# Kernel tuning notes

Measured on AMD Instinct MI355X. Metric: run time of the kernel, lower is better.

## Reference

```python
import jax, jax.numpy as jnp
import numpy as np

HIDDEN = 1024
HEADS = 16
HEAD_DIM = HIDDEN // HEADS
EPS = 1e-6


def _layernorm(x, gamma, beta):
    mu = jnp.mean(x, axis=-1, keepdims=True)
    var = jnp.mean(jnp.square(x - mu), axis=-1, keepdims=True)
    return (x - mu) * jax.lax.rsqrt(var + EPS) * gamma + beta


def setup_inputs() -> dict:
    key = jax.random.key(0)
    ks = jax.random.split(key, 16)
    B, S, D = 2, 2048, HIDDEN
    s = 1.0 / np.sqrt(D)
    inp = {
        "x": jax.random.normal(ks[0], (B, S, D), dtype=jnp.float32),
        "Wq": jax.random.uniform(ks[1], (D, D), jnp.float32, -s, s),
        "bq": jnp.zeros((D,), jnp.float32),
        "Wk": jax.random.uniform(ks[2], (D, D), jnp.float32, -s, s),
        "bk": jnp.zeros((D,), jnp.float32),
        "Wv": jax.random.uniform(ks[3], (D, D), jnp.float32, -s, s),
        "bv": jnp.zeros((D,), jnp.float32),
        "Wo": jax.random.uniform(ks[4], (D, D), jnp.float32, -s, s),
        "bo": jnp.zeros((D,), jnp.float32),
        "g1": jnp.ones((D,), jnp.float32),
        "b1": jnp.zeros((D,), jnp.float32),
        "Wup": jax.random.uniform(ks[5], (D, 4 * D), jnp.float32, -s, s),
        "bup": jnp.zeros((4 * D,), jnp.float32),
        "Wdn": jax.random.uniform(ks[6], (4 * D, D), jnp.float32, -0.5 * s, 0.5 * s),
        "bdn": jnp.zeros((D,), jnp.float32),
        "g2": jnp.ones((D,), jnp.float32),
        "b2": jnp.zeros((D,), jnp.float32),
    }
    return inp


def _forward(x, Wq, bq, Wk, bk, Wv, bv, Wo, bo, g1, b1, Wup, bup, Wdn, bdn, g2, b2):
    B, S, D = x.shape
    H, Hd = HEADS, HEAD_DIM
    # projections -> (B, H, S, Hd)
    q = (x @ Wq + bq).reshape(B, S, H, Hd).transpose(0, 2, 1, 3)
    k = (x @ Wk + bk).reshape(B, S, H, Hd).transpose(0, 2, 1, 3)
    v = (x @ Wv + bv).reshape(B, S, H, Hd).transpose(0, 2, 1, 3)
    # full NxN scores (faithful to the source: explicit QK^T, mask, softmax, AV)
    scores = jnp.einsum("bhqd,bhkd->bhqk", q, k) / np.sqrt(Hd)
    causal = jnp.tril(jnp.ones((S, S), dtype=bool))  # (S, S)
    scores = jnp.where(causal, scores, jnp.float32(-1e20))
    attn = jax.nn.softmax(scores, axis=-1)
    # dropout is identity in eval mode
    mid = jnp.einsum("bhqk,bhkd->bqhd", attn, v).reshape(B, S, D)
    attn_out = mid @ Wo + bo
    x = _layernorm(x + attn_out, g1, b1)
    # FFN
    up = jax.nn.relu(x @ Wup + bup)
    down = up @ Wdn + bdn
    return _layernorm(x + down, g2, b2)


def reference(x, Wq, bq, Wk, bk, Wv, bv, Wo, bo, g1, b1, Wup, bup, Wdn, bdn, g2, b2):
    return _forward(x, Wq, bq, Wk, bk, Wv, bv, Wo, bo, g1, b1, Wup, bup, Wdn, bdn, g2, b2)
```

## Files before the change

kernel.cpp:

```cpp
#include <hip/hip_runtime.h>

#define D_MODEL 1024
#define D_FFN   4096
#define SEQ     2048
#define NROWS   4096
#define QKV_LD  3072

typedef __bf16 bf16x8 __attribute__((ext_vector_type(8)));
typedef float  floatx4 __attribute__((ext_vector_type(4)));

#define MFMA_BF16 __builtin_amdgcn_mfma_f32_16x16x32_bf16

__device__ __forceinline__ unsigned short f2bf(float f) {
  unsigned int u = __float_as_uint(f);
  u += 0x7FFFu + ((u >> 16) & 1u);
  return (unsigned short)(u >> 16);
}

template <int C>
__device__ __forceinline__ float ror16(float x) {
  return __int_as_float(
      __builtin_amdgcn_mov_dpp(__float_as_int(x), 0x120 | C, 0xf, 0xf, true));
}

__device__ __forceinline__ void async16(const unsigned short* g, unsigned short* l) {
  __builtin_amdgcn_global_load_lds(
      (const __attribute__((address_space(1))) unsigned int*)g,
      (__attribute__((address_space(3))) unsigned int*)l, 16, 0, 0);
}

__global__ __launch_bounds__(256) void k_f32_to_bf16(
    const float* __restrict__ in, unsigned short* __restrict__ outp, long n) {
  long i = ((long)blockIdx.x * 256 + threadIdx.x) * 4;
  if (i >= n) return;
  float4 v = *(const float4*)(in + i);
  ushort4 o;
  o.x = f2bf(v.x); o.y = f2bf(v.y); o.z = f2bf(v.z); o.w = f2bf(v.w);
  *(ushort4*)(outp + i) = o;
}

__global__ __launch_bounds__(256) void k_transpose_bf16(
    const float* __restrict__ W, unsigned short* __restrict__ WT, int R, int C) {
  __shared__ float tile[32][33];
  int tx = threadIdx.x & 31, ty = threadIdx.x >> 5;
  long bx = (long)blockIdx.x * 32;
  long by = (long)blockIdx.y * 32;
  #pragma unroll
  for (int j = 0; j < 4; j++)
    tile[ty + j * 8][tx] = W[(by + ty + j * 8) * C + bx + tx];
  __syncthreads();
  #pragma unroll
  for (int j = 0; j < 4; j++)
    WT[(bx + ty + j * 8) * R + by + tx] = f2bf(tile[tx][ty + j * 8]);
}

__global__ __launch_bounds__(256) void k_transpose_sq(
    const float* __restrict__ Wq, const float* __restrict__ Wk,
    const float* __restrict__ Wv, const float* __restrict__ Wo,
    unsigned short* __restrict__ WqkvT, unsigned short* __restrict__ WoT) {
  __shared__ float tile[32][33];
  int z = blockIdx.z;
  const float* W = (z == 0) ? Wq : (z == 1) ? Wk : (z == 2) ? Wv : Wo;
  unsigned short* dst = (z < 3) ? (WqkvT + (size_t)z * D_MODEL * D_MODEL) : WoT;
  int tx = threadIdx.x & 31, ty = threadIdx.x >> 5;
  long bx = (long)blockIdx.x * 32;
  long by = (long)blockIdx.y * 32;
  #pragma unroll
  for (int j = 0; j < 4; j++)
    tile[ty + j * 8][tx] = W[(by + ty + j * 8) * D_MODEL + bx + tx];
  __syncthreads();
  #pragma unroll
  for (int j = 0; j < 4; j++)
    dst[(bx + ty + j * 8) * D_MODEL + by + tx] = f2bf(tile[tx][ty + j * 8]);
}

__global__ __launch_bounds__(256) void k_pack_bias(
    const float* __restrict__ bq, const float* __restrict__ bk,
    const float* __restrict__ bv, float* __restrict__ dst) {
  int i = blockIdx.x * 256 + threadIdx.x;
  if (i >= 3072) return;
  float v = (i < 1024) ? bq[i] : (i < 2048) ? bk[i - 1024] : bv[i - 2048];
  dst[i] = v;
}

__global__ __launch_bounds__(256) void k_transpose_v(
    const unsigned short* __restrict__ QKV, unsigned short* __restrict__ Vt) {
  __shared__ unsigned short tile[64][72];
  int r0 = blockIdx.x * 64;
  int c0 = blockIdx.y * 64;
  int tx = threadIdx.x & 15, ty = threadIdx.x >> 4;
  #pragma unroll
  for (int j = 0; j < 4; j++) {
    int r = ty + j * 16;
    *(ushort4*)&tile[r][tx * 4] =
        *(const ushort4*)(QKV + (long)(r0 + r) * QKV_LD + 2048 + c0 + tx * 4);
  }
  __syncthreads();
  #pragma unroll
  for (int j = 0; j < 4; j++) {
    int d = ty + j * 16;
    ushort4 o;
    o.x = tile[tx * 4 + 0][d];
    o.y = tile[tx * 4 + 1][d];
    o.z = tile[tx * 4 + 2][d];
    o.w = tile[tx * 4 + 3][d];
    *(ushort4*)(Vt + (long)(c0 + d) * NROWS + r0 + tx * 4) = o;
  }
}

__global__ __launch_bounds__(512, 4) void k_gemm128(
    const unsigned short* __restrict__ A,
    const unsigned short* __restrict__ Bt,
    const float* __restrict__ bias,
    void* __restrict__ Cp, int M, int N, int K, int flags) {
  __shared__ unsigned short lds[2 * 16384];
  int tid = threadIdx.x, lane = tid & 63, wave = tid >> 6;
  int quad = lane >> 4, l16 = lane & 15;
  int wm = wave >> 2, wn = wave & 3;

  int gx = gridDim.x;
  int nwg = gx * gridDim.y;
  int orig = blockIdx.y * gx + blockIdx.x;
  int wg = (orig & 7) * (nwg >> 3) + (orig >> 3);
  long bm = (long)(wg % gx) * 128;
  long bn = (long)(wg / gx) * 128;

  int T = K / 64;

  const floatx4 fz = {0.f, 0.f, 0.f, 0.f};
  floatx4 acc[4][2];
  #pragma unroll
  for (int i = 0; i < 4; i++)
    #pragma unroll
    for (int j = 0; j < 2; j++) acc[i][j] = fz;

  int srow = tid >> 3;
  int sc = (tid & 7) ^ (srow & 7);
  const unsigned short* Ag = A + (bm + srow) * (long)K + sc * 8;
  const unsigned short* Bg = Bt + (bn + srow) * (long)K + sc * 8;

  auto stage = [&](int tt, int c) {
    unsigned short* An = lds + c * 16384;
    unsigned short* Bn = An + 8192;
    long ko = (long)tt * 64;
    async16(Ag + ko, An + wave * 512);
    async16(Ag + 64 * (long)K + ko, An + 4096 + wave * 512);
    async16(Bg + ko, Bn + wave * 512);
    async16(Bg + 64 * (long)K + ko, Bn + 4096 + wave * 512);
  };

  int aoff = (wm * 64 + l16) * 64;
  int boff = (wn * 32 + l16) * 64;
  int sw = l16 & 7;
  int ca0 = (quad ^ sw) * 8;
  int ca1 = ((4 + quad) ^ sw) * 8;

  stage(0, 0);
  for (int t = 0; t < T; t++) {
    int c = t & 1;
    const unsigned short* Ac = lds + c * 16384;
    const unsigned short* Bc = Ac + 8192;
    int tn = (t + 1 < T) ? t + 1 : T - 1;
    stage(tn, c ^ 1);
    __asm__ volatile("s_waitcnt vmcnt(4)" ::: "memory");
    __builtin_amdgcn_s_barrier();

    bf16x8 af[4][2], bfr[2][2];
    #pragma unroll
    for (int m = 0; m < 4; m++) {
      af[m][0] = *(const bf16x8*)(Ac + aoff + m * 1024 + ca0);
      af[m][1] = *(const bf16x8*)(Ac + aoff + m * 1024 + ca1);
    }
    #pragma unroll
    for (int n = 0; n < 2; n++) {
      bfr[n][0] = *(const bf16x8*)(Bc + boff + n * 1024 + ca0);
      bfr[n][1] = *(const bf16x8*)(Bc + boff + n * 1024 + ca1);
    }
    __asm__ volatile("s_waitcnt lgkmcnt(0)" ::: "memory");
    __builtin_amdgcn_s_setprio(1);
    #pragma unroll
    for (int h = 0; h < 2; h++)
      #pragma unroll
      for (int m = 0; m < 4; m++)
        #pragma unroll
        for (int n = 0; n < 2; n++)
          acc[m][n] = MFMA_BF16(af[m][h], bfr[n][h], acc[m][n], 0, 0, 0);
    __builtin_amdgcn_s_setprio(0);
    __builtin_amdgcn_s_barrier();
  }

  bool f32out = (flags & 1) != 0;
  bool relu   = (flags & 2) != 0;
  float* outf = (float*)Cp;
  unsigned short* outh = (unsigned short*)Cp;
  #pragma unroll
  for (int n = 0; n < 2; n++) {
    long col = bn + wn * 32 + n * 16 + l16;
    float bvv = bias[col];
    #pragma unroll
    for (int m = 0; m < 4; m++) {
      long row = bm + wm * 64 + m * 16 + quad * 4;
      #pragma unroll
      for (int r = 0; r < 4; r++) {
        float v = acc[m][n][r] + bvv;
        if (relu) v = fmaxf(v, 0.0f);
        if (f32out) outf[(row + r) * (long)N + col] = v;
        else        outh[(row + r) * (long)N + col] = f2bf(v);
      }
    }
  }
}

__global__ __launch_bounds__(512, 2) void k_gemm256(
    const unsigned short* __restrict__ A,
    const unsigned short* __restrict__ Bt,
    const float* __restrict__ bias,
    void* __restrict__ Cp, int M, int N, int K, int flags) {
  extern __shared__ unsigned short lds[];
  int tid = threadIdx.x, lane = tid & 63, wave = tid >> 6;
  int quad = lane >> 4, l16 = lane & 15;
  int wm = wave >> 2, wn = wave & 3;

  int nwg = gridDim.x * gridDim.y;
  int orig = blockIdx.y * gridDim.x + blockIdx.x;
  int wg = (orig & 7) * (nwg >> 3) + (orig >> 3);
  long bm = (long)(wg & 15) * 256;
  long bn = (long)(wg >> 4) * 256;

  int z = blockIdx.z;
  int Ks = K / gridDim.z;
  long zb = (long)z * Ks;
  int T = Ks / 64;

  const floatx4 fz = {0.f, 0.f, 0.f, 0.f};
  floatx4 acc[8][4];
  #pragma unroll
  for (int i = 0; i < 8; i++)
    #pragma unroll
    for (int j = 0; j < 4; j++) acc[i][j] = fz;

  int srow = tid >> 3;
  int sc = (tid & 7) ^ (srow & 7);
  const unsigned short* Ag = A + (bm + srow) * (long)K + zb + sc * 8;
  const unsigned short* Bg = Bt + (bn + srow) * (long)K + zb + sc * 8;

  auto stage = [&](int tt, int c) {
    unsigned short* An = lds + c * 32768;
    unsigned short* Bn = An + 16384;
    long ko = (long)tt * 64;
    #pragma unroll
    for (int i = 0; i < 4; i++) {
      async16(Ag + (long)i * 64 * K + ko, An + i * 4096 + wave * 512);
      async16(Bg + (long)i * 64 * K + ko, Bn + i * 4096 + wave * 512);
    }
  };

  int aoff = (wm * 128 + l16) * 64;
  int boff = (wn * 64 + l16) * 64;
  int sw = l16 & 7;
  int ca0 = (quad ^ sw) * 8;
  int ca1 = ((4 + quad) ^ sw) * 8;

  stage(0, 0);
  for (int t = 0; t < T; t++) {
    int c = t & 1;
    const unsigned short* Ac = lds + c * 32768;
    const unsigned short* Bc = Ac + 16384;
    int tn = (t + 1 < T) ? t + 1 : T - 1;
    stage(tn, c ^ 1);
    __asm__ volatile("s_waitcnt vmcnt(8)" ::: "memory");
    __builtin_amdgcn_s_barrier();

    bf16x8 af[8], b0, b1;
    #pragma unroll
    for (int m = 0; m < 8; m++) af[m] = *(const bf16x8*)(Ac + aoff + m * 1024 + ca0);
    b0 = *(const bf16x8*)(Bc + boff + 0 * 1024 + ca0);
    b1 = *(const bf16x8*)(Bc + boff + 1 * 1024 + ca0);
    __asm__ volatile("s_waitcnt lgkmcnt(0)" ::: "memory");
    __builtin_amdgcn_s_setprio(1);
    #pragma unroll
    for (int m = 0; m < 8; m++) acc[m][0] = MFMA_BF16(af[m], b0, acc[m][0], 0, 0, 0);
    #pragma unroll
    for (int m = 0; m < 8; m++) acc[m][1] = MFMA_BF16(af[m], b1, acc[m][1], 0, 0, 0);
    __builtin_amdgcn_s_setprio(0);
    __builtin_amdgcn_s_barrier();
    b0 = *(const bf16x8*)(Bc + boff + 2 * 1024 + ca0);
    b1 = *(const bf16x8*)(Bc + boff + 3 * 1024 + ca0);
    __asm__ volatile("s_waitcnt lgkmcnt(0)" ::: "memory");
    __builtin_amdgcn_s_setprio(1);
    #pragma unroll
    for (int m = 0; m < 8; m++) acc[m][2] = MFMA_BF16(af[m], b0, acc[m][2], 0, 0, 0);
    #pragma unroll
    for (int m = 0; m < 8; m++) acc[m][3] = MFMA_BF16(af[m], b1, acc[m][3], 0, 0, 0);
    __builtin_amdgcn_s_setprio(0);
    __builtin_amdgcn_s_barrier();
    #pragma unroll
    for (int m = 0; m < 8; m++) af[m] = *(const bf16x8*)(Ac + aoff + m * 1024 + ca1);
    b0 = *(const bf16x8*)(Bc + boff + 0 * 1024 + ca1);
    b1 = *(const bf16x8*)(Bc + boff + 1 * 1024 + ca1);
    __asm__ volatile("s_waitcnt lgkmcnt(0)" ::: "memory");
    __builtin_amdgcn_s_setprio(1);
    #pragma unroll
    for (int m = 0; m < 8; m++) acc[m][0] = MFMA_BF16(af[m], b0, acc[m][0], 0, 0, 0);
    #pragma unroll
    for (int m = 0; m < 8; m++) acc[m][1] = MFMA_BF16(af[m], b1, acc[m][1], 0, 0, 0);
    __builtin_amdgcn_s_setprio(0);
    __builtin_amdgcn_s_barrier();
    b0 = *(const bf16x8*)(Bc + boff + 2 * 1024 + ca1);
    b1 = *(const bf16x8*)(Bc + boff + 3 * 1024 + ca1);
    __asm__ volatile("s_waitcnt lgkmcnt(0)" ::: "memory");
    __builtin_amdgcn_s_setprio(1);
    #pragma unroll
    for (int m = 0; m < 8; m++) acc[m][2] = MFMA_BF16(af[m], b0, acc[m][2], 0, 0, 0);
    #pragma unroll
    for (int m = 0; m < 8; m++) acc[m][3] = MFMA_BF16(af[m], b1, acc[m][3], 0, 0, 0);
    __builtin_amdgcn_s_setprio(0);
    __builtin_amdgcn_s_barrier();
  }

  bool f32out = (flags & 1) != 0;
  bool relu   = (flags & 2) != 0;
  float* outf = (float*)Cp + (size_t)z * M * (size_t)N;
  unsigned short* outh = (unsigned short*)Cp;
  #pragma unroll
  for (int n = 0; n < 4; n++) {
    long col = bn + wn * 64 + n * 16 + l16;
    float bvv = (z == 0) ? bias[col] : 0.0f;
    #pragma unroll
    for (int m = 0; m < 8; m++) {
      long row = bm + wm * 128 + m * 16 + quad * 4;
      #pragma unroll
      for (int r = 0; r < 4; r++) {
        float v = acc[m][n][r] + bvv;
        if (relu) v = fmaxf(v, 0.0f);
        if (f32out) outf[(row + r) * (long)N + col] = v;
        else        outh[(row + r) * (long)N + col] = f2bf(v);
      }
    }
  }
}

#define PLD 72
__global__ __launch_bounds__(256) void k_attn(
    const unsigned short* __restrict__ QKV,
    const unsigned short* __restrict__ Vt,
    unsigned short* __restrict__ Omat) {
  __shared__ unsigned short Ks[64 * 64];
  __shared__ unsigned short Vs[64 * 64];
  __shared__ unsigned short Ps[4][16 * PLD];
  int tid = threadIdx.x;
  int lane = tid & 63, wave = tid >> 6;
  int quad = lane >> 4, l16 = lane & 15;
  int z = blockIdx.x;
  int bh = z & 31;
  int qt = 31 - (z >> 5);
  int b = bh >> 4, h = bh & 15;
  long rowbase = (long)b * SEQ;
  int hd0 = h * 64;
  unsigned short* pw = &Ps[wave][0];
  const float SCL = 0.18033688f;
  const floatx4 fz = {0.f, 0.f, 0.f, 0.f};

  int r_in = lane >> 3;
  int cpos = lane & 7;

  bf16x8 ones;
  #pragma unroll
  for (int i = 0; i < 8; i++) ones[i] = (__bf16)1.0f;

  int q0w = qt * 64 + wave * 16;
  int qrow = q0w + quad * 4;
  int ntiles = qt + 1;

  bf16x8 qf0, qf1;
  {
    const unsigned short* qp_ =
        QKV + (rowbase + q0w + l16) * (long)QKV_LD + hd0 + quad * 8;
    qf0 = *(const bf16x8*)(qp_);
    qf1 = *(const bf16x8*)(qp_ + 32);
  }

  floatx4 ao[4], aol;
  #pragma unroll
  for (int t = 0; t < 4; t++) ao[t] = fz;
  aol = fz;
  float m_i[4];
  #pragma unroll
  for (int r = 0; r < 4; r++) m_i[r] = -3.0e38f;

  for (int it = 0; it < ntiles; it++) {
    int kv0 = it << 6;
    #pragma unroll
    for (int jj = 0; jj < 2; jj++) {
      int j = wave * 2 + jj;
      int r = j * 8 + r_in;
      int c = cpos ^ (r & 7);
      const unsigned short* gk =
          QKV + (rowbase + kv0 + r) * (long)QKV_LD + 1024 + hd0 + c * 8;
      async16(gk, Ks + j * 512);
      const unsigned short* gv =
          Vt + (long)(hd0 + r) * NROWS + rowbase + kv0 + c * 8;
      async16(gv, Vs + j * 512);
    }
    __syncthreads();

    floatx4 sacc[4];
    #pragma unroll
    for (int t = 0; t < 4; t++) {
      int row = t * 16 + l16;
      int sw = row & 7;
      bf16x8 kf0 = *(const bf16x8*)(Ks + row * 64 + (quad ^ sw) * 8);
      bf16x8 kf1 = *(const bf16x8*)(Ks + row * 64 + ((quad + 4) ^ sw) * 8);
      sacc[t] = __builtin_amdgcn_mfma_f32_16x16x32_bf16(qf0, kf0, fz, 0, 0, 0);
      sacc[t] = __builtin_amdgcn_mfma_f32_16x16x32_bf16(qf1, kf1, sacc[t], 0, 0, 0);
    }

    if (it == ntiles - 1) {
      #pragma unroll
      for (int t = 0; t < 4; t++) {
        int kvc = kv0 + t * 16 + l16;
        #pragma unroll
        for (int r = 0; r < 4; r++)
          sacc[t][r] = (kvc > qrow + r) ? -1.0e30f : sacc[t][r];
      }
    }

    float Mg = sacc[0][0];
    #pragma unroll
    for (int t = 0; t < 4; t++)
      #pragma unroll
      for (int r = 0; r < 4; r++) Mg = fmaxf(Mg, sacc[t][r]);
    Mg = fmaxf(Mg, ror16<1>(Mg));
    Mg = fmaxf(Mg, ror16<2>(Mg));
    Mg = fmaxf(Mg, ror16<4>(Mg));
    Mg = fmaxf(Mg, ror16<8>(Mg));
    float Mg_s = Mg * SCL;

    float m_min = fminf(fminf(m_i[0], m_i[1]), fminf(m_i[2], m_i[3]));
    if (Mg_s > m_min + 8.0f) {
      #pragma unroll
      for (int r = 0; r < 4; r++) {
        float mn = fmaxf(m_i[r], Mg_s);
        float alpha = __builtin_amdgcn_exp2f(m_i[r] - mn);
        m_i[r] = mn;
        #pragma unroll
        for (int t = 0; t < 4; t++) ao[t][r] *= alpha;
        aol[r] *= alpha;
      }
    }

    #pragma unroll
    for (int t = 0; t < 4; t++)
      #pragma unroll
      for (int r = 0; r < 4; r++) {
        float p = __builtin_amdgcn_exp2f(fmaf(sacc[t][r], SCL, -m_i[r]));
        pw[(quad * 4 + r) * PLD + t * 16 + l16] =
            (unsigned short)(__float_as_uint(p) >> 16);
      }

    __asm__ volatile("s_waitcnt lgkmcnt(0)" ::: "memory");
    bf16x8 pf0 = *(const bf16x8*)(pw + l16 * PLD + quad * 8);
    bf16x8 pf1 = *(const bf16x8*)(pw + l16 * PLD + 32 + quad * 8);

    #pragma unroll
    for (int t = 0; t < 4; t++) {
      int row = t * 16 + l16;
      int sw = row & 7;
      bf16x8 vf0 = *(const bf16x8*)(Vs + row * 64 + (quad ^ sw) * 8);
      bf16x8 vf1 = *(const bf16x8*)(Vs + row * 64 + ((quad + 4) ^ sw) * 8);
      ao[t] = __builtin_amdgcn_mfma_f32_16x16x32_bf16(pf0, vf0, ao[t], 0, 0, 0);
      ao[t] = __builtin_amdgcn_mfma_f32_16x16x32_bf16(pf1, vf1, ao[t], 0, 0, 0);
    }
    aol = __builtin_amdgcn_mfma_f32_16x16x32_bf16(pf0, ones, aol, 0, 0, 0);
    aol = __builtin_amdgcn_mfma_f32_16x16x32_bf16(pf1, ones, aol, 0, 0, 0);

    __syncthreads();
  }

  float inv[4];
  #pragma unroll
  for (int r = 0; r < 4; r++) inv[r] = 1.0f / aol[r];
  #pragma unroll
  for (int t = 0; t < 4; t++)
    #pragma unroll
    for (int r = 0; r < 4; r++)
      Omat[(rowbase + qrow + r) * (long)D_MODEL + hd0 + t * 16 + l16] =
          f2bf(ao[t][r] * inv[r]);
}

__global__ __launch_bounds__(256) void k_add_ln(
    const float* __restrict__ A, const float* __restrict__ P,
    const float* __restrict__ g, const float* __restrict__ be,
    float* __restrict__ Y, unsigned short* __restrict__ Ybf) {
  __shared__ float sb[4], ssb[4];
  int tid = threadIdx.x;
  long base = (long)blockIdx.x * D_MODEL + tid * 4;
  float4 a  = *(const float4*)(A + base);
  float4 p0 = *(const float4*)(P + base);
  float v0 = a.x + p0.x;
  float v1 = a.y + p0.y;
  float v2 = a.z + p0.z;
  float v3 = a.w + p0.w;
  float s  = v0 + v1 + v2 + v3;
  float ss = v0 * v0 + v1 * v1 + v2 * v2 + v3 * v3;
  #pragma unroll
  for (int o = 32; o >= 1; o >>= 1) {
    s  += __shfl_xor(s, o, 64);
    ss += __shfl_xor(ss, o, 64);
  }
  int wave = tid >> 6;
  if ((tid & 63) == 0) { sb[wave] = s; ssb[wave] = ss; }
  __syncthreads();
  s  = sb[0] + sb[1] + sb[2] + sb[3];
  ss = ssb[0] + ssb[1] + ssb[2] + ssb[3];
  float mu  = s * (1.0f / 1024.0f);
  float var = ss * (1.0f / 1024.0f) - mu * mu;
  float rstd = rsqrtf(var + 1e-6f);
  float4 gv  = *(const float4*)(g + tid * 4);
  float4 bev = *(const float4*)(be + tid * 4);
  float o0 = (v0 - mu) * rstd * gv.x + bev.x;
  float o1 = (v1 - mu) * rstd * gv.y + bev.y;
  float o2 = (v2 - mu) * rstd * gv.z + bev.z;
  float o3 = (v3 - mu) * rstd * gv.w + bev.w;
  if (Y) *(float4*)(Y + base) = make_float4(o0, o1, o2, o3);
  if (Ybf) {
    ushort4 u;
    u.x = f2bf(o0); u.y = f2bf(o1); u.z = f2bf(o2); u.w = f2bf(o3);
    *(ushort4*)(Ybf + base) = u;
  }
}

extern "C" void kernel_launch(void* const* d_in, const int* in_sizes, int n_in,
                              void* d_out, int out_size, void* d_ws, size_t ws_size,
                              hipStream_t stream) {
  (void)in_sizes; (void)n_in; (void)out_size; (void)ws_size;
  static bool s_attr = false;
  if (!s_attr) {
    hipFuncSetAttribute((const void*)k_gemm256,
                        hipFuncAttributeMaxDynamicSharedMemorySize, 131072);
    s_attr = true;
  }
  const float* x   = (const float*)d_in[0];
  const float* Wq  = (const float*)d_in[1];
  const float* bq  = (const float*)d_in[2];
  const float* Wk  = (const float*)d_in[3];
  const float* bk  = (const float*)d_in[4];
  const float* Wv  = (const float*)d_in[5];
  const float* bv  = (const float*)d_in[6];
  const float* Wo  = (const float*)d_in[7];
  const float* bo  = (const float*)d_in[8];
  const float* g1  = (const float*)d_in[9];
  const float* b1  = (const float*)d_in[10];
  const float* Wup = (const float*)d_in[11];
  const float* bup = (const float*)d_in[12];
  const float* Wdn = (const float*)d_in[13];
  const float* bdn = (const float*)d_in[14];
  const float* g2  = (const float*)d_in[15];
  const float* b2  = (const float*)d_in[16];
  float* out = (float*)d_out;

  char* ws = (char*)d_ws;
  size_t off = 0;
  auto alloc = [&](size_t bytes) {
    char* p = ws + off;
    off = (off + bytes + 255) & ~(size_t)255;
    return p;
  };
  unsigned short* x_bf   = (unsigned short*)alloc((size_t)NROWS * D_MODEL * 2);
  unsigned short* WqkvT  = (unsigned short*)alloc((size_t)QKV_LD * D_MODEL * 2);
  unsigned short* WoT    = (unsigned short*)alloc((size_t)D_MODEL * D_MODEL * 2);
  unsigned short* WupT   = (unsigned short*)alloc((size_t)D_FFN * D_MODEL * 2);
  unsigned short* WdnT   = (unsigned short*)alloc((size_t)D_MODEL * D_FFN * 2);
  float*          bqkv   = (float*)alloc((size_t)QKV_LD * 4);
  unsigned short* qkv_bf = (unsigned short*)alloc((size_t)NROWS * QKV_LD * 2);
  unsigned short* Vt     = (unsigned short*)alloc((size_t)D_MODEL * NROWS * 2);
  unsigned short* mid_bf = (unsigned short*)alloc((size_t)NROWS * D_MODEL * 2);
  float*          x1f    = (float*)alloc((size_t)NROWS * D_MODEL * 4);
  unsigned short* x1bf   = (unsigned short*)alloc((size_t)NROWS * D_MODEL * 2);
  float*          part   = (float*)alloc((size_t)NROWS * D_MODEL * 4);
  unsigned short* h_bf   = (unsigned short*)alloc((size_t)NROWS * D_FFN * 2);

  k_f32_to_bf16<<<4096, 256, 0, stream>>>(x, x_bf, (long)NROWS * D_MODEL);
  k_transpose_sq<<<dim3(32, 32, 4), 256, 0, stream>>>(Wq, Wk, Wv, Wo, WqkvT, WoT);
  k_transpose_bf16<<<dim3(128, 32), 256, 0, stream>>>(Wup, WupT, D_MODEL, D_FFN);
  k_transpose_bf16<<<dim3(32, 128), 256, 0, stream>>>(Wdn, WdnT, D_FFN, D_MODEL);
  k_pack_bias<<<12, 256, 0, stream>>>(bq, bk, bv, bqkv);

  k_gemm128<<<dim3(32, 24), 512, 0, stream>>>(x_bf, WqkvT, bqkv, qkv_bf,
                                              NROWS, QKV_LD, D_MODEL, 0);
  k_transpose_v<<<dim3(64, 16), 256, 0, stream>>>(qkv_bf, Vt);

  k_attn<<<1024, 256, 0, stream>>>(qkv_bf, Vt, mid_bf);

  k_gemm128<<<dim3(32, 8), 512, 0, stream>>>(mid_bf, WoT, bo, part,
                                             NROWS, D_MODEL, D_MODEL, 1);
  k_add_ln<<<4096, 256, 0, stream>>>(x, part, g1, b1, x1f, x1bf);

  k_gemm256<<<dim3(16, 16, 1), 512, 131072, stream>>>(x1bf, WupT, bup, h_bf,
                                                      NROWS, D_FFN, D_MODEL, 2);
  k_gemm128<<<dim3(32, 8), 512, 0, stream>>>(h_bf, WdnT, bdn, part,
                                             NROWS, D_MODEL, D_FFN, 1);
  k_add_ln<<<4096, 256, 0, stream>>>(x1f, part, g2, b2, out, nullptr);
}
```

Baseline: 372.0 us.

## Replace 256-tile FFN-up GEMM with 128-tile kernel and LDS-staged bf16 stores

Removes the 256x256-tile k_gemm256 kernel and runs the FFN up-projection with the 128-tile k_gemm128 kernel on a 32x32 grid. The bf16 output path of k_gemm128 now stages each wave's results through LDS so global stores become 16-byte vectorised row writes instead of scattered 2-byte stores. This affects the QKV and FFN-up GEMMs. The cost is an extra barrier and an LDS round trip in the epilogue, plus lower per-block data reuse for the FFN-up GEMM.

```diff
diff --git a/kernel.cpp b/kernel.cpp
--- a/kernel.cpp
+++ b/kernel.cpp
@@ -191,151 +191,51 @@
 
   bool f32out = (flags & 1) != 0;
   bool relu   = (flags & 2) != 0;
-  float* outf = (float*)Cp;
-  unsigned short* outh = (unsigned short*)Cp;
-  #pragma unroll
-  for (int n = 0; n < 2; n++) {
-    long col = bn + wn * 32 + n * 16 + l16;
-    float bvv = bias[col];
-    #pragma unroll
-    for (int m = 0; m < 4; m++) {
-      long row = bm + wm * 64 + m * 16 + quad * 4;
-      #pragma unroll
-      for (int r = 0; r < 4; r++) {
-        float v = acc[m][n][r] + bvv;
-        if (relu) v = fmaxf(v, 0.0f);
-        if (f32out) outf[(row + r) * (long)N + col] = v;
-        else        outh[(row + r) * (long)N + col] = f2bf(v);
+  if (f32out) {
+    float* outf = (float*)Cp;
+    #pragma unroll
+    for (int n = 0; n < 2; n++) {
+      long col = bn + wn * 32 + n * 16 + l16;
+      float bvv = bias[col];
+      #pragma unroll
+      for (int m = 0; m < 4; m++) {
+        long row = bm + wm * 64 + m * 16 + quad * 4;
+        #pragma unroll
+        for (int r = 0; r < 4; r++) {
+          float v = acc[m][n][r] + bvv;
+          if (relu) v = fmaxf(v, 0.0f);
+          outf[(row + r) * (long)N + col] = v;
+        }
       }
     }
-  }
-}
-
-__global__ __launch_bounds__(512, 2) void k_gemm256(
-    const unsigned short* __restrict__ A,
-    const unsigned short* __restrict__ Bt,
-    const float* __restrict__ bias,
-    void* __restrict__ Cp, int M, int N, int K, int flags) {
-  extern __shared__ unsigned short lds[];
-  int tid = threadIdx.x, lane = tid & 63, wave = tid >> 6;
-  int quad = lane >> 4, l16 = lane & 15;
-  int wm = wave >> 2, wn = wave & 3;
-
-  int nwg = gridDim.x * gridDim.y;
-  int orig = blockIdx.y * gridDim.x + blockIdx.x;
-  int wg = (orig & 7) * (nwg >> 3) + (orig >> 3);
-  long bm = (long)(wg & 15) * 256;
-  long bn = (long)(wg >> 4) * 256;
-
-  int z = blockIdx.z;
-  int Ks = K / gridDim.z;
-  long zb = (long)z * Ks;
-  int T = Ks / 64;
-
-  const floatx4 fz = {0.f, 0.f, 0.f, 0.f};
-  floatx4 acc[8][4];
-  #pragma unroll
-  for (int i = 0; i < 8; i++)
-    #pragma unroll
-    for (int j = 0; j < 4; j++) acc[i][j] = fz;
-
-  int srow = tid >> 3;
-  int sc = (tid & 7) ^ (srow & 7);
-  const unsigned short* Ag = A + (bm + srow) * (long)K + zb + sc * 8;
-  const unsigned short* Bg = Bt + (bn + srow) * (long)K + zb + sc * 8;
-
-  auto stage = [&](int tt, int c) {
-    unsigned short* An = lds + c * 32768;
-    unsigned short* Bn = An + 16384;
-    long ko = (long)tt * 64;
-    #pragma unroll
-    for (int i = 0; i < 4; i++) {
-      async16(Ag + (long)i * 64 * K + ko, An + i * 4096 + wave * 512);
-      async16(Bg + (long)i * 64 * K + ko, Bn + i * 4096 + wave * 512);
-    }
-  };
-
-  int aoff = (wm * 128 + l16) * 64;
-  int boff = (wn * 64 + l16) * 64;
-  int sw = l16 & 7;
-  int ca0 = (quad ^ sw) * 8;
-  int ca1 = ((4 + quad) ^ sw) * 8;
-
-  stage(0, 0);
-  for (int t = 0; t < T; t++) {
-    int c = t & 1;
-    const unsigned short* Ac = lds + c * 32768;
-    const unsigned short* Bc = Ac + 16384;
-    int tn = (t + 1 < T) ? t + 1 : T - 1;
-    stage(tn, c ^ 1);
-    __asm__ volatile("s_waitcnt vmcnt(8)" ::: "memory");
-    __builtin_amdgcn_s_barrier();
-
-    bf16x8 af[8], b0, b1;
-    #pragma unroll
-    for (int m = 0; m < 8; m++) af[m] = *(const bf16x8*)(Ac + aoff + m * 1024 + ca0);
-    b0 = *(const bf16x8*)(Bc + boff + 0 * 1024 + ca0);
-    b1 = *(const bf16x8*)(Bc + boff + 1 * 1024 + ca0);
-    __asm__ volatile("s_waitcnt lgkmcnt(0)" ::: "memory");
-    __builtin_amdgcn_s_setprio(1);
-    #pragma unroll
-    for (int m = 0; m < 8; m++) acc[m][0] = MFMA_BF16(af[m], b0, acc[m][0], 0, 0, 0);
-    #pragma unroll
-    for (int m = 0; m < 8; m++) acc[m][1] = MFMA_BF16(af[m], b1, acc[m][1], 0, 0, 0);
-    __builtin_amdgcn_s_setprio(0);
-    __builtin_amdgcn_s_barrier();
-    b0 = *(const bf16x8*)(Bc + boff + 2 * 1024 + ca0);
-    b1 = *(const bf16x8*)(Bc + boff + 3 * 1024 + ca0);
-    __asm__ volatile("s_waitcnt lgkmcnt(0)" ::: "memory");
-    __builtin_amdgcn_s_setprio(1);
-    #pragma unroll
-    for (int m = 0; m < 8; m++) acc[m][2] = MFMA_BF16(af[m], b0, acc[m][2], 0, 0, 0);
-    #pragma unroll
-    for (int m = 0; m < 8; m++) acc[m][3] = MFMA_BF16(af[m], b1, acc[m][3], 0, 0, 0);
-    __builtin_amdgcn_s_setprio(0);
-    __builtin_amdgcn_s_barrier();
-    #pragma unroll
-    for (int m = 0; m < 8; m++) af[m] = *(const bf16x8*)(Ac + aoff + m * 1024 + ca1);
-    b0 = *(const bf16x8*)(Bc + boff + 0 * 1024 + ca1);
-    b1 = *(const bf16x8*)(Bc + boff + 1 * 1024 + ca1);
-    __asm__ volatile("s_waitcnt lgkmcnt(0)" ::: "memory");
-    __builtin_amdgcn_s_setprio(1);
-    #pragma unroll
-    for (int m = 0; m < 8; m++) acc[m][0] = MFMA_BF16(af[m], b0, acc[m][0], 0, 0, 0);
-    #pragma unroll
-    for (int m = 0; m < 8; m++) acc[m][1] = MFMA_BF16(af[m], b1, acc[m][1], 0, 0, 0);
-    __builtin_amdgcn_s_setprio(0);
-    __builtin_amdgcn_s_barrier();
-    b0 = *(const bf16x8*)(Bc + boff + 2 * 1024 + ca1);
-    b1 = *(const bf16x8*)(Bc + boff + 3 * 1024 + ca1);
-    __asm__ volatile("s_waitcnt lgkmcnt(0)" ::: "memory");
-    __builtin_amdgcn_s_setprio(1);
-    #pragma unroll
-    for (int m = 0; m < 8; m++) acc[m][2] = MFMA_BF16(af[m], b0, acc[m][2], 0, 0, 0);
-    #pragma unroll
-    for (int m = 0; m < 8; m++) acc[m][3] = MFMA_BF16(af[m], b1, acc[m][3], 0, 0, 0);
-    __builtin_amdgcn_s_setprio(0);
-    __builtin_amdgcn_s_barrier();
-  }
-
-  bool f32out = (flags & 1) != 0;
-  bool relu   = (flags & 2) != 0;
-  float* outf = (float*)Cp + (size_t)z * M * (size_t)N;
-  unsigned short* outh = (unsigned short*)Cp;
-  #pragma unroll
-  for (int n = 0; n < 4; n++) {
-    long col = bn + wn * 64 + n * 16 + l16;
-    float bvv = (z == 0) ? bias[col] : 0.0f;
-    #pragma unroll
-    for (int m = 0; m < 8; m++) {
-      long row = bm + wm * 128 + m * 16 + quad * 4;
-      #pragma unroll
-      for (int r = 0; r < 4; r++) {
-        float v = acc[m][n][r] + bvv;
-        if (relu) v = fmaxf(v, 0.0f);
-        if (f32out) outf[(row + r) * (long)N + col] = v;
-        else        outh[(row + r) * (long)N + col] = f2bf(v);
+  } else {
+    __asm__ volatile("s_waitcnt vmcnt(0)" ::: "memory");
+    __syncthreads();
+    unsigned short* outh = (unsigned short*)Cp;
+    unsigned short* lw = lds + wave * 2560;
+    #pragma unroll
+    for (int n = 0; n < 2; n++) {
+      long col = bn + wn * 32 + n * 16 + l16;
+      float bvv = bias[col];
+      #pragma unroll
+      for (int m = 0; m < 4; m++) {
+        #pragma unroll
+        for (int r = 0; r < 4; r++) {
+          float v = acc[m][n][r] + bvv;
+          if (relu) v = fmaxf(v, 0.0f);
+          lw[(m * 16 + quad * 4 + r) * 40 + n * 16 + l16] = f2bf(v);
+        }
       }
+    }
+    int rrb = lane >> 2;
+    int c8 = (lane & 3) * 8;
+    long grow = bm + wm * 64;
+    long gcol = bn + wn * 32 + c8;
+    #pragma unroll
+    for (int k = 0; k < 4; k++) {
+      int rr = rrb + k * 16;
+      bf16x8 vv = *(const bf16x8*)(lw + rr * 40 + c8);
+      *(bf16x8*)(outh + (grow + rr) * (long)N + gcol) = vv;
     }
   }
 }
@@ -534,12 +434,6 @@
                               void* d_out, int out_size, void* d_ws, size_t ws_size,
                               hipStream_t stream) {
   (void)in_sizes; (void)n_in; (void)out_size; (void)ws_size;
-  static bool s_attr = false;
-  if (!s_attr) {
-    hipFuncSetAttribute((const void*)k_gemm256,
-                        hipFuncAttributeMaxDynamicSharedMemorySize, 131072);
-    s_attr = true;
-  }
   const float* x   = (const float*)d_in[0];
   const float* Wq  = (const float*)d_in[1];
   const float* bq  = (const float*)d_in[2];
@@ -596,8 +490,8 @@
                                              NROWS, D_MODEL, D_MODEL, 1);
   k_add_ln<<<4096, 256, 0, stream>>>(x, part, g1, b1, x1f, x1bf);
 
-  k_gemm256<<<dim3(16, 16, 1), 512, 131072, stream>>>(x1bf, WupT, bup, h_bf,
-                                                      NROWS, D_FFN, D_MODEL, 2);
+  k_gemm128<<<dim3(32, 32), 512, 0, stream>>>(x1bf, WupT, bup, h_bf,
+                                              NROWS, D_FFN, D_MODEL, 2);
   k_gemm128<<<dim3(32, 8), 512, 0, stream>>>(h_bf, WdnT, bdn, part,
                                              NROWS, D_MODEL, D_FFN, 1);
   k_add_ln<<<4096, 256, 0, stream>>>(x1f, part, g2, b2, out, nullptr);
```

After: 346.6 us. 1.07x faster.
